# Kernel optimization log

Hardware: AMD Instinct MI355X
Metric: run time of the kernel (lower is better)

## Reference

```python
import jax, jax.numpy as jnp
import numpy as np

N = 20000
E = 640000


def setup_inputs() -> dict:
    key = jax.random.key(0)
    k1, k2, k3, k4 = jax.random.split(key, 4)
    IN, H, C = 4096, 512, 10
    x = jax.random.normal(k1, (N, IN), dtype=jnp.float32)
    edge_index = jax.random.randint(k2, (2, E), 0, N, dtype=jnp.int64)
    W1 = jax.random.normal(k3, (IN, H), dtype=jnp.float32) * (1.0 / np.sqrt(IN))
    b1 = jnp.zeros((H,), dtype=jnp.float32)
    W2 = jax.random.normal(k4, (H, C), dtype=jnp.float32) * (1.0 / np.sqrt(H))
    b2 = jnp.zeros((C,), dtype=jnp.float32)
    return {"x": x, "edge_index": edge_index, "W1": W1, "b1": b1, "W2": W2, "b2": b2}


def _gcn_conv(x, src, dst, W, b):
    # Dense transform first (PyG GCNConv does XW then propagate).
    h = x @ W  # [N, F_out]
    # Add self loops.
    loops = jnp.arange(N, dtype=src.dtype)
    s = jnp.concatenate([src, loops])
    d = jnp.concatenate([dst, loops])
    # Symmetric normalization D^{-1/2} (A+I) D^{-1/2}; degree counted on dst.
    deg = jax.ops.segment_sum(jnp.ones_like(d, dtype=h.dtype), d, num_segments=N)
    dinv = jnp.where(deg > 0, jax.lax.rsqrt(deg), 0.0)
    norm = dinv[s] * dinv[d]  # [E+N]
    msg = h[s] * norm[:, None]  # gather + scale
    out = jax.ops.segment_sum(msg, d, num_segments=N)  # scatter-add aggregate
    return out + b


def reference(x, edge_index, W1, b1, W2, b2):
    src, dst = edge_index[0], edge_index[1]
    h = _gcn_conv(x, src, dst, W1, b1)  # conv1 (dropout disabled / eval)
    h = jax.nn.relu(h)
    h = _gcn_conv(h, src, dst, W2, b2)  # conv2
    return jax.nn.log_softmax(h, axis=1)
```

## Files before the change

### kernel.cpp

```cpp
#include <hip/hip_runtime.h>
#include <cstdint>
#include <cstddef>

#define NN  20000
#define EE  640000
#define KIN 4096
#define HD  512
#define NC  10
#define CAP 128

typedef __attribute__((ext_vector_type(8))) short short8;
typedef __attribute__((ext_vector_type(4))) float f32x4;

__device__ __forceinline__ unsigned short f2b(float f) {
  union { float f; unsigned int u; } v; v.f = f;
  unsigned int r = v.u + 0x7fffu + ((v.u >> 16) & 1u);
  return (unsigned short)(r >> 16);
}

__device__ __forceinline__ unsigned int cvt2(float lo, float hi) {
  unsigned int r;
  asm("v_cvt_pk_bf16_f32 %0, %1, %2" : "=v"(r) : "v"(lo), "v"(hi));
  return r;
}

__device__ __forceinline__ void gload16(const void* g, void* l) {
  __builtin_amdgcn_global_load_lds(
      (const __attribute__((address_space(1))) unsigned int*)g,
      (__attribute__((address_space(3))) unsigned int*)l, 16, 0, 0);
}

__global__ __launch_bounds__(256) void scatk(const int* __restrict__ src, const int* __restrict__ dst,
                                             int* __restrict__ deg, int* __restrict__ csr) {
  int e = blockIdx.x * 256 + threadIdx.x;
  if (e < EE) {
    int d = dst[e];
    int p = atomicAdd(&deg[d], 1);
    csr[d * CAP + p] = src[e];
  }
}

__global__ __launch_bounds__(256) void dinvk(const int* __restrict__ deg, float* __restrict__ dinv) {
  int i = blockIdx.x * 256 + threadIdx.x;
  if (i < NN) dinv[i] = 1.0f / sqrtf((float)(deg[i] + 1));
}

__global__ __launch_bounds__(256) void transk(const float* __restrict__ W1, unsigned short* __restrict__ w1t) {
  __shared__ float tile[32][33];
  int h0 = blockIdx.x * 32;
  int k0 = blockIdx.y * 32;
  int tx = threadIdx.x & 31, ty = threadIdx.x >> 5;
#pragma unroll
  for (int r = 0; r < 4; ++r) {
    int k = ty * 4 + r;
    tile[k][tx] = W1[(size_t)(k0 + k) * HD + h0 + tx];
  }
  __syncthreads();
#pragma unroll
  for (int r = 0; r < 4; ++r) {
    int h = ty * 4 + r;
    w1t[(size_t)(h0 + h) * KIN + k0 + tx] = f2b(tile[tx][h]);
  }
}

__global__ __launch_bounds__(256) void gemm1(const float* __restrict__ x,
                                             const unsigned short* __restrict__ w1t,
                                             unsigned short* __restrict__ h1b) {
  __shared__ __align__(16) unsigned short As[2][128 * 64];
  __shared__ __align__(16) unsigned short Bs[2][128 * 64];
  int t = threadIdx.x;
  int l = t & 63, w = t >> 6;
  int wm = w >> 1, wn = w & 1;

  int orig = blockIdx.x;
  int xcd = orig & 7, jj = orig >> 3;
  int tile = (xcd < 4 ? xcd * 79 : 316 + (xcd - 4) * 78) + jj;
  int bm = (tile >> 2) * 128;
  int bn = (tile & 3) * 128;

  int stRow = t >> 3;
  int stQ = (t & 7) ^ (stRow & 7);
  const float* ga[4];
#pragma unroll
  for (int i = 0; i < 4; ++i) {
    int m = bm + i * 32 + stRow;
    if (m > NN - 1) m = NN - 1;
    ga[i] = x + (size_t)m * KIN + stQ * 8;
  }

  int rl = l >> 3;
  int cq = (l & 7) ^ rl;
  const unsigned short* gb[4];
  int lBoff[4];
#pragma unroll
  for (int i = 0; i < 4; ++i) {
    int rowB = bn + i * 32 + w * 8 + rl;
    gb[i] = w1t + (size_t)rowB * KIN + cq * 8;
    lBoff[i] = (i * 32 + w * 8) * 64;
  }

  int col0 = ((l >> 4) ^ (l & 7));
  int fm[4], fn[4];
#pragma unroll
  for (int i = 0; i < 4; ++i) fm[i] = (wm * 64 + i * 16 + (l & 15)) * 64 + col0 * 8;
#pragma unroll
  for (int j = 0; j < 4; ++j) fn[j] = (wn * 64 + j * 16 + (l & 15)) * 64 + col0 * 8;

  f32x4 acc[4][4] = {};
  float4 pa[4][2];

#pragma unroll
  for (int i = 0; i < 4; ++i) {
    pa[i][0] = *reinterpret_cast<const float4*>(ga[i]);
    pa[i][1] = *reinterpret_cast<const float4*>(ga[i] + 4);
  }
#pragma unroll
  for (int i = 0; i < 4; ++i) gload16(gb[i], &Bs[0][lBoff[i]]);
#pragma unroll
  for (int i = 0; i < 4; ++i) {
    uint4 val;
    val.x = cvt2(pa[i][0].x, pa[i][0].y);
    val.y = cvt2(pa[i][0].z, pa[i][0].w);
    val.z = cvt2(pa[i][1].x, pa[i][1].y);
    val.w = cvt2(pa[i][1].z, pa[i][1].w);
    *reinterpret_cast<uint4*>(&As[0][i * 2048 + 8 * t]) = val;
  }
  __syncthreads();

  for (int tk = 0; tk < 64; ++tk) {
    int cur = tk & 1;
    int k1 = (tk + 1) * 64;
    if (tk < 63) {
#pragma unroll
      for (int i = 0; i < 4; ++i) {
        pa[i][0] = *reinterpret_cast<const float4*>(ga[i] + k1);
        pa[i][1] = *reinterpret_cast<const float4*>(ga[i] + k1 + 4);
      }
#pragma unroll
      for (int i = 0; i < 4; ++i) gload16(gb[i] + k1, &Bs[cur ^ 1][lBoff[i]]);
    }
#pragma unroll
    for (int kk = 0; kk < 2; ++kk) {
      int xr = kk << 5;
      short8 af[4], bf[4];
#pragma unroll
      for (int i = 0; i < 4; ++i) af[i] = *reinterpret_cast<const short8*>(&As[cur][0] + (fm[i] ^ xr));
#pragma unroll
      for (int j = 0; j < 4; ++j) bf[j] = *reinterpret_cast<const short8*>(&Bs[cur][0] + (fn[j] ^ xr));
#pragma unroll
      for (int i = 0; i < 4; ++i)
#pragma unroll
        for (int j = 0; j < 4; ++j)
          acc[i][j] = __builtin_amdgcn_mfma_f32_16x16x32_bf16(af[i], bf[j], acc[i][j], 0, 0, 0);
    }
    if (tk < 63) {
#pragma unroll
      for (int i = 0; i < 4; ++i) {
        uint4 val;
        val.x = cvt2(pa[i][0].x, pa[i][0].y);
        val.y = cvt2(pa[i][0].z, pa[i][0].w);
        val.z = cvt2(pa[i][1].x, pa[i][1].y);
        val.w = cvt2(pa[i][1].z, pa[i][1].w);
        *reinterpret_cast<uint4*>(&As[cur ^ 1][i * 2048 + 8 * t]) = val;
      }
      __syncthreads();
    }
  }

  int lq = l >> 4;
  bool even = (l & 1) == 0;
#pragma unroll
  for (int i = 0; i < 4; ++i) {
    int row0 = bm + wm * 64 + i * 16 + lq * 4;
#pragma unroll
    for (int j = 0; j < 4; ++j) {
      int col = bn + wn * 64 + j * 16 + (l & 15);
#pragma unroll
      for (int r = 0; r < 4; ++r) {
        float v0 = acc[i][j][r];
        float v1 = __shfl_xor(v0, 1);
        int row = row0 + r;
        if (even && row < NN) {
          *reinterpret_cast<unsigned int*>(h1b + (size_t)row * HD + col) = cvt2(v0, v1);
        }
      }
    }
  }
}

__global__ __launch_bounds__(256) void sgk(const unsigned short* __restrict__ h1b, const int* __restrict__ deg,
                                           const int* __restrict__ csr, const float* __restrict__ dinv,
                                           const float* __restrict__ b1, const float* __restrict__ W2,
                                           float* __restrict__ h2) {
  __shared__ int s_idx[CAP];
  __shared__ float s_w[CAP];
  __shared__ float red[4][NC];
  int i = blockIdx.x;
  int c = threadIdx.x;
  float di = dinv[i];
  int dg = deg[i];
  if (c < dg) {
    int s = csr[i * CAP + c];
    s_idx[c] = s;
    s_w[c] = dinv[s] * di;
  }
  const unsigned int* h1v = reinterpret_cast<const unsigned int*>(h1b);
  unsigned int su = h1v[(size_t)i * 256 + c];
  float wself = di * di;
  float a0 = __uint_as_float(su << 16) * wself;
  float a1 = __uint_as_float(su & 0xffff0000u) * wself;
  __syncthreads();
#pragma unroll 4
  for (int jj = 0; jj < dg; ++jj) {
    unsigned int u = h1v[(size_t)s_idx[jj] * 256 + c];
    float wgt = s_w[jj];
    a0 += __uint_as_float(u << 16) * wgt;
    a1 += __uint_as_float(u & 0xffff0000u) * wgt;
  }
  float2 bb = reinterpret_cast<const float2*>(b1)[c];
  float zx = fmaxf(a0 + bb.x, 0.f);
  float zy = fmaxf(a1 + bb.y, 0.f);
  const float* w2r = W2 + (size_t)(2 * c) * NC;
  float part[NC];
#pragma unroll
  for (int cc = 0; cc < NC; ++cc) part[cc] = zx * w2r[cc] + zy * w2r[NC + cc];
#pragma unroll
  for (int cc = 0; cc < NC; ++cc) {
#pragma unroll
    for (int m = 1; m < 64; m <<= 1) part[cc] += __shfl_xor(part[cc], m, 64);
  }
  int wv = c >> 6, ln = c & 63;
  if (ln == 0) {
#pragma unroll
    for (int cc = 0; cc < NC; ++cc) red[wv][cc] = part[cc];
  }
  __syncthreads();
  if (c < NC) h2[(size_t)i * NC + c] = red[0][c] + red[1][c] + red[2][c] + red[3][c];
}

__global__ __launch_bounds__(64) void spmm2(const float* __restrict__ h2, const int* __restrict__ deg,
                                            const int* __restrict__ csr, const float* __restrict__ dinv,
                                            const float* __restrict__ b2, float* __restrict__ out) {
  int i = blockIdx.x;
  int l = threadIdx.x;
  float di = dinv[i];
  int dg = deg[i];
  float acc[NC] = {};
  for (int e = l; e < dg; e += 64) {
    int s = csr[i * CAP + e];
    float wgt = dinv[s] * di;
    const float2* hp = reinterpret_cast<const float2*>(h2 + (size_t)s * NC);
#pragma unroll
    for (int cc = 0; cc < 5; ++cc) {
      float2 v = hp[cc];
      acc[2 * cc] += v.x * wgt;
      acc[2 * cc + 1] += v.y * wgt;
    }
  }
  if (l == 0) {
    float ws = di * di;
#pragma unroll
    for (int cc = 0; cc < NC; ++cc) acc[cc] += h2[(size_t)i * NC + cc] * ws;
  }
#pragma unroll
  for (int cc = 0; cc < NC; ++cc) {
#pragma unroll
    for (int m = 1; m < 64; m <<= 1) acc[cc] += __shfl_xor(acc[cc], m, 64);
  }
  if (l == 0) {
    float v[NC];
    float mx = -1e30f;
#pragma unroll
    for (int cc = 0; cc < NC; ++cc) {
      v[cc] = acc[cc] + b2[cc];
      mx = fmaxf(mx, v[cc]);
    }
    float s = 0.f;
#pragma unroll
    for (int cc = 0; cc < NC; ++cc) s += expf(v[cc] - mx);
    float lse = mx + logf(s);
#pragma unroll
    for (int cc = 0; cc < NC; ++cc) out[(size_t)i * NC + cc] = v[cc] - lse;
  }
}

extern "C" void kernel_launch(void* const* d_in, const int* in_sizes, int n_in,
                              void* d_out, int out_size, void* d_ws, size_t ws_size,
                              hipStream_t stream) {
  (void)in_sizes; (void)n_in; (void)out_size; (void)ws_size;
  const float* x  = (const float*)d_in[0];
  const int*   ei = (const int*)d_in[1];
  const float* W1 = (const float*)d_in[2];
  const float* b1 = (const float*)d_in[3];
  const float* W2 = (const float*)d_in[4];
  const float* b2 = (const float*)d_in[5];
  float* out = (float*)d_out;
  char* ws = (char*)d_ws;

  unsigned short* w1t = (unsigned short*)(ws);
  unsigned short* h1b = (unsigned short*)(ws + 4194304);
  float* h2   = (float*)(ws + 24674304);
  int*   deg  = (int*)(ws + 25474304);
  float* dinv = (float*)(ws + 25554304);
  int*   csr  = (int*)(ws + 25634304);

  const int* srcp = ei;
  const int* dstp = ei + EE;

  hipMemsetAsync(deg, 0, NN * sizeof(int), stream);
  scatk<<<(EE + 255) / 256, 256, 0, stream>>>(srcp, dstp, deg, csr);
  dinvk<<<(NN + 255) / 256, 256, 0, stream>>>(deg, dinv);
  transk<<<dim3(16, 128), 256, 0, stream>>>(W1, w1t);
  gemm1<<<157 * 4, 256, 0, stream>>>(x, w1t, h1b);
  sgk<<<NN, 256, 0, stream>>>(h1b, deg, csr, dinv, b1, W2, h2);
  spmm2<<<NN, 64, 0, stream>>>(h2, deg, csr, dinv, b2, out);
}
```

Before: 758.2 us.

## Single-buffer A tile in gemm1 and widen sgk gather to uint2 per thread

```diff
diff --git a/kernel.cpp b/kernel.cpp
--- a/kernel.cpp
+++ b/kernel.cpp
@@ -29,6 +29,9 @@
       (const __attribute__((address_space(1))) unsigned int*)g,
       (__attribute__((address_space(3))) unsigned int*)l, 16, 0, 0);
 }
+
+__device__ __forceinline__ float bflo(unsigned int u) { return __uint_as_float(u << 16); }
+__device__ __forceinline__ float bfhi(unsigned int u) { return __uint_as_float(u & 0xffff0000u); }
 
 __global__ __launch_bounds__(256) void scatk(const int* __restrict__ src, const int* __restrict__ dst,
                                              int* __restrict__ deg, int* __restrict__ csr) {
@@ -66,7 +69,7 @@
 __global__ __launch_bounds__(256) void gemm1(const float* __restrict__ x,
                                              const unsigned short* __restrict__ w1t,
                                              unsigned short* __restrict__ h1b) {
-  __shared__ __align__(16) unsigned short As[2][128 * 64];
+  __shared__ __align__(16) unsigned short As[128 * 64];
   __shared__ __align__(16) unsigned short Bs[2][128 * 64];
   int t = threadIdx.x;
   int l = t & 63, w = t >> 6;
@@ -123,14 +126,14 @@
     val.y = cvt2(pa[i][0].z, pa[i][0].w);
     val.z = cvt2(pa[i][1].x, pa[i][1].y);
     val.w = cvt2(pa[i][1].z, pa[i][1].w);
-    *reinterpret_cast<uint4*>(&As[0][i * 2048 + 8 * t]) = val;
+    *reinterpret_cast<uint4*>(&As[i * 2048 + 8 * t]) = val;
   }
   __syncthreads();
 
   for (int tk = 0; tk < 64; ++tk) {
     int cur = tk & 1;
-    int k1 = (tk + 1) * 64;
     if (tk < 63) {
+      int k1 = (tk + 1) * 64;
 #pragma unroll
       for (int i = 0; i < 4; ++i) {
         pa[i][0] = *reinterpret_cast<const float4*>(ga[i] + k1);
@@ -139,12 +142,13 @@
 #pragma unroll
       for (int i = 0; i < 4; ++i) gload16(gb[i] + k1, &Bs[cur ^ 1][lBoff[i]]);
     }
+    __builtin_amdgcn_sched_barrier(0);
 #pragma unroll
     for (int kk = 0; kk < 2; ++kk) {
       int xr = kk << 5;
       short8 af[4], bf[4];
 #pragma unroll
-      for (int i = 0; i < 4; ++i) af[i] = *reinterpret_cast<const short8*>(&As[cur][0] + (fm[i] ^ xr));
+      for (int i = 0; i < 4; ++i) af[i] = *reinterpret_cast<const short8*>(As + (fm[i] ^ xr));
 #pragma unroll
       for (int j = 0; j < 4; ++j) bf[j] = *reinterpret_cast<const short8*>(&Bs[cur][0] + (fn[j] ^ xr));
 #pragma unroll
@@ -153,7 +157,10 @@
         for (int j = 0; j < 4; ++j)
           acc[i][j] = __builtin_amdgcn_mfma_f32_16x16x32_bf16(af[i], bf[j], acc[i][j], 0, 0, 0);
     }
+    __builtin_amdgcn_sched_barrier(0);
     if (tk < 63) {
+      __builtin_amdgcn_s_barrier();
+      __builtin_amdgcn_sched_barrier(0);
 #pragma unroll
       for (int i = 0; i < 4; ++i) {
         uint4 val;
@@ -161,7 +168,7 @@
         val.y = cvt2(pa[i][0].z, pa[i][0].w);
         val.z = cvt2(pa[i][1].x, pa[i][1].y);
         val.w = cvt2(pa[i][1].z, pa[i][1].w);
-        *reinterpret_cast<uint4*>(&As[cur ^ 1][i * 2048 + 8 * t]) = val;
+        *reinterpret_cast<uint4*>(&As[i * 2048 + 8 * t]) = val;
       }
       __syncthreads();
     }
@@ -188,13 +195,13 @@
   }
 }
 
-__global__ __launch_bounds__(256) void sgk(const unsigned short* __restrict__ h1b, const int* __restrict__ deg,
+__global__ __launch_bounds__(128) void sgk(const unsigned short* __restrict__ h1b, const int* __restrict__ deg,
                                            const int* __restrict__ csr, const float* __restrict__ dinv,
                                            const float* __restrict__ b1, const float* __restrict__ W2,
                                            float* __restrict__ h2) {
   __shared__ int s_idx[CAP];
   __shared__ float s_w[CAP];
-  __shared__ float red[4][NC];
+  __shared__ float red[2][NC];
   int i = blockIdx.x;
   int c = threadIdx.x;
   float di = dinv[i];
@@ -204,26 +211,31 @@
     s_idx[c] = s;
     s_w[c] = dinv[s] * di;
   }
-  const unsigned int* h1v = reinterpret_cast<const unsigned int*>(h1b);
-  unsigned int su = h1v[(size_t)i * 256 + c];
+  const uint2* h1v = reinterpret_cast<const uint2*>(h1b);
+  uint2 su = h1v[(size_t)i * 128 + c];
   float wself = di * di;
-  float a0 = __uint_as_float(su << 16) * wself;
-  float a1 = __uint_as_float(su & 0xffff0000u) * wself;
+  float a0 = bflo(su.x) * wself, a1 = bfhi(su.x) * wself;
+  float a2 = bflo(su.y) * wself, a3 = bfhi(su.y) * wself;
   __syncthreads();
 #pragma unroll 4
   for (int jj = 0; jj < dg; ++jj) {
-    unsigned int u = h1v[(size_t)s_idx[jj] * 256 + c];
+    uint2 u = h1v[(size_t)s_idx[jj] * 128 + c];
     float wgt = s_w[jj];
-    a0 += __uint_as_float(u << 16) * wgt;
-    a1 += __uint_as_float(u & 0xffff0000u) * wgt;
-  }
-  float2 bb = reinterpret_cast<const float2*>(b1)[c];
-  float zx = fmaxf(a0 + bb.x, 0.f);
-  float zy = fmaxf(a1 + bb.y, 0.f);
-  const float* w2r = W2 + (size_t)(2 * c) * NC;
+    a0 += bflo(u.x) * wgt;
+    a1 += bfhi(u.x) * wgt;
+    a2 += bflo(u.y) * wgt;
+    a3 += bfhi(u.y) * wgt;
+  }
+  float4 bb = reinterpret_cast<const float4*>(b1)[c];
+  float z0 = fmaxf(a0 + bb.x, 0.f);
+  float z1 = fmaxf(a1 + bb.y, 0.f);
+  float z2 = fmaxf(a2 + bb.z, 0.f);
+  float z3 = fmaxf(a3 + bb.w, 0.f);
+  const float* w2r = W2 + (size_t)(4 * c) * NC;
   float part[NC];
 #pragma unroll
-  for (int cc = 0; cc < NC; ++cc) part[cc] = zx * w2r[cc] + zy * w2r[NC + cc];
+  for (int cc = 0; cc < NC; ++cc)
+    part[cc] = z0 * w2r[cc] + z1 * w2r[NC + cc] + z2 * w2r[2 * NC + cc] + z3 * w2r[3 * NC + cc];
 #pragma unroll
   for (int cc = 0; cc < NC; ++cc) {
 #pragma unroll
@@ -235,7 +247,7 @@
     for (int cc = 0; cc < NC; ++cc) red[wv][cc] = part[cc];
   }
   __syncthreads();
-  if (c < NC) h2[(size_t)i * NC + c] = red[0][c] + red[1][c] + red[2][c] + red[3][c];
+  if (c < NC) h2[(size_t)i * NC + c] = red[0][c] + red[1][c];
 }
 
 __global__ __launch_bounds__(64) void spmm2(const float* __restrict__ h2, const int* __restrict__ deg,
@@ -312,6 +324,6 @@
   dinvk<<<(NN + 255) / 256, 256, 0, stream>>>(deg, dinv);
   transk<<<dim3(16, 128), 256, 0, stream>>>(W1, w1t);
   gemm1<<<157 * 4, 256, 0, stream>>>(x, w1t, h1b);
-  sgk<<<NN, 256, 0, stream>>>(h1b, deg, csr, dinv, b1, W2, h2);
+  sgk<<<NN, 128, 0, stream>>>(h1b, deg, csr, dinv, b1, W2, h2);
   spmm2<<<NN, 64, 0, stream>>>(h2, deg, csr, dinv, b2, out);
 }
```

Result: faster. 706.3 us (-6.8%).
